# Optimization experiments

Measured on AMD Instinct MI355X. Metric: run time of the kernel, lower is better.

## Reference

```python
import jax, jax.numpy as jnp
import numpy as np

B = 32; H = 56; W = 56; C = 384; NH = 12; WS = 14; SS = 7
L = H * W; N = WS * WS; HD = C // NH; SCALE = HD ** -0.5; HID = 4 * C
NW = (H // WS) * (W // WS)
EPS = 1e-5

def _relative_index():
    ch = np.arange(WS)[:, None].repeat(WS, 1)
    cw = np.arange(WS)[None, :].repeat(WS, 0)
    coords = np.stack([ch, cw], -1).reshape(-1, 2)  # [N,2]
    rel = coords[:, None, :] - coords[None, :, :]
    rel = rel + (WS - 1)
    rel[:, :, 0] *= 2 * WS - 1
    return rel.sum(-1)  # [N,N], values in [0,(2WS-1)^2)

def _attn_mask():
    img = np.zeros((H, W))
    sl = (slice(0, -WS), slice(-WS, -SS), slice(-SS, None))
    cnt = 0
    for hs in sl:
        for ws_ in sl:
            img[hs, ws_] = cnt; cnt += 1
    mw = img.reshape(H // WS, WS, W // WS, WS).transpose(0, 2, 1, 3).reshape(-1, N)
    am = mw[:, None, :] - mw[:, :, None]  # [nW,N,N]
    return np.where(am != 0, -100.0, 0.0).astype(np.float32)

REL_IDX = jnp.asarray(_relative_index())
MASK = jnp.asarray(_attn_mask())  # [NW,N,N]

def _ln(x, w, b):
    m = jnp.mean(x, -1, keepdims=True)
    v = jnp.mean((x - m) ** 2, -1, keepdims=True)
    return (x - m) * jax.lax.rsqrt(v + EPS) * w + b

def setup_inputs() -> dict:
    key = jax.random.key(0)
    ks = jax.random.split(key, 8)
    s = 0.02
    return {
        "x": jax.random.normal(ks[0], (B, L, C), jnp.float32),
        "norm1_w": jnp.ones((C,), jnp.float32),
        "norm1_b": jnp.zeros((C,), jnp.float32),
        "qkv_w": jax.random.normal(ks[1], (3 * C, C), jnp.float32) * s,
        "qkv_b": jnp.zeros((3 * C,), jnp.float32),
        "proj_w": jax.random.normal(ks[2], (C, C), jnp.float32) * s,
        "proj_b": jnp.zeros((C,), jnp.float32),
        "relative_table": jax.random.normal(ks[3], ((2 * WS - 1) ** 2, 2 * NH), jnp.float32) * s,
        "norm2_w": jnp.ones((C,), jnp.float32),
        "norm2_b": jnp.zeros((C,), jnp.float32),
        "fc1_w": jax.random.normal(ks[4], (HID, C), jnp.float32) * s,
        "fc1_b": jnp.zeros((HID,), jnp.float32),
        "fc2_w": jax.random.normal(ks[5], (C, HID), jnp.float32) * s,
        "fc2_b": jnp.zeros((C,), jnp.float32),
    }

def reference(x, norm1_w, norm1_b, qkv_w, qkv_b, proj_w, proj_b,
              relative_table, norm2_w, norm2_b, fc1_w, fc1_b, fc2_w, fc2_b):
    shortcut = x
    xn = _ln(x, norm1_w, norm1_b).reshape(B, H, W, C)
    # cyclic shift + window partition -> [B*NW, N, C]
    xs = jnp.roll(xn, (-SS, -SS), (1, 2))
    xw = xs.reshape(B, H // WS, WS, W // WS, WS, C).transpose(0, 1, 3, 2, 4, 5).reshape(-1, N, C)
    B_ = B * NW
    qkv = (xw @ qkv_w.T + qkv_b).reshape(B_, N, 3, NH, HD).transpose(2, 0, 3, 1, 4)
    q, k, v = qkv[0] * SCALE, qkv[1], qkv[2]  # [B_,NH,N,HD]
    attn = jnp.einsum('bhnd,bhmd->bhnm', q, k)  # [B_,NH,N,N]
    rel = relative_table[REL_IDX]  # [N,N,2*NH]
    rel = rel.transpose(2, 0, 1)  # [2*NH,N,N]
    bias, rscale = rel[:NH], rel[NH:]
    attn = attn + bias[None]
    attn = attn.reshape(B, NW, NH, N, N) + MASK[None, :, None]
    attn = jax.nn.softmax(attn.reshape(B_, NH, N, N), axis=-1)
    attn = attn * rscale[None]  # multiplicative relative scale AFTER softmax
    out = jnp.einsum('bhnm,bhmd->bhnd', attn, v)
    out = out.transpose(0, 2, 1, 3).reshape(B_, N, C)
    out = out @ proj_w.T + proj_b
    # window reverse + reverse shift
    xr = out.reshape(B, H // WS, W // WS, WS, WS, C).transpose(0, 1, 3, 2, 4, 5).reshape(B, H, W, C)
    xr = jnp.roll(xr, (SS, SS), (1, 2)).reshape(B, L, C)
    x = shortcut + xr
    h = _ln(x, norm2_w, norm2_b)
    h = jax.nn.gelu(h @ fc1_w.T + fc1_b, approximate=False) @ fc2_w.T + fc2_b
    return x + h
```

## Files before the change

### kernel.cpp

```cpp
#include <hip/hip_runtime.h>
#include <hip/hip_bf16.h>
#include <math.h>

#define BDIM 32
#define HDIM 56
#define WDIM 56
#define CDIM 384
#define NHEAD 12
#define WSZ 14
#define SSZ 7
#define LDIM (HDIM*WDIM)
#define NTOK (WSZ*WSZ)
#define HDHEAD (CDIM/NHEAD)
#define HIDDIM (4*CDIM)
#define NWIN 16
#define BWIN (BDIM*NWIN)
#define MROWS (BDIM*LDIM)
#define EPSLN 1e-5f
#define ATTSCALE 0.17677669529663687f
#define QKVC (3*CDIM)

#define KROW 40
#define VROW 232
#define PROW 232

typedef __hip_bfloat16 bf16;
typedef __attribute__((ext_vector_type(8))) short bf16x8;
typedef __attribute__((ext_vector_type(4))) short s16x4;
typedef __attribute__((ext_vector_type(4))) float f32x4;

#define ASYNC16(gp, lp) __builtin_amdgcn_global_load_lds( \
    (__attribute__((address_space(1))) void*)(gp),        \
    (__attribute__((address_space(3))) void*)(lp), 16, 0, 0)

static __device__ __forceinline__ short f2bfs(float x) {
  union { bf16 h; short s; } u; u.h = __float2bfloat16(x); return u.s;
}
static __device__ __forceinline__ float bfs2f(short s) {
  unsigned int u = ((unsigned int)(unsigned short)s) << 16;
  float f; __builtin_memcpy(&f, &u, 4); return f;
}
static __device__ __forceinline__ float tof(float x) { return x; }
static __device__ __forceinline__ float tof(bf16 x)  { return __bfloat162float(x); }

__global__ __launch_bounds__(256) void k_cvt(const float* __restrict__ in,
                                             bf16* __restrict__ out, int n)
{
  int i = blockIdx.x * 256 + threadIdx.x;
  if (i < n) out[i] = __float2bfloat16(in[i]);
}

template<bool WIN, typename TIN>
__global__ __launch_bounds__(128) void k_ln(const TIN* __restrict__ xin,
    const float* __restrict__ gw, const float* __restrict__ gb,
    bf16* __restrict__ out)
{
  int r = blockIdx.x;
  int t = threadIdx.x;
  const TIN* xp = xin + (size_t)r * CDIM;
  float v0 = tof(xp[t]), v1 = tof(xp[t+128]), v2 = tof(xp[t+256]);
  float s  = v0+v1+v2;
  float ss = v0*v0 + v1*v1 + v2*v2;
  #pragma unroll
  for (int o = 32; o > 0; o >>= 1) { s += __shfl_down(s, o); ss += __shfl_down(ss, o); }
  __shared__ float red[4];
  if ((t & 63) == 0) { red[(t>>6)*2] = s; red[(t>>6)*2+1] = ss; }
  __syncthreads();
  float mean = (red[0]+red[2]) * (1.0f/CDIM);
  float var  = (red[1]+red[3]) * (1.0f/CDIM) - mean*mean;
  float rstd = rsqrtf(var + EPSLN);

  size_t orow;
  if (WIN) {
    int b = r / LDIM, l = r % LDIM;
    int h = l / WDIM, w = l % WDIM;
    int h2 = (h + HDIM - SSZ) % HDIM, w2 = (w + WDIM - SSZ) % WDIM;
    int wh = h2 / WSZ, ii = h2 % WSZ, ww = w2 / WSZ, jj = w2 % WSZ;
    int b_ = b*NWIN + wh*4 + ww;
    int n  = ii*WSZ + jj;
    orow = ((size_t)b_*NTOK + n) * CDIM;
  } else {
    orow = (size_t)r * CDIM;
  }
  out[orow+t]     = __float2bfloat16((v0-mean)*rstd*gw[t]     + gb[t]);
  out[orow+t+128] = __float2bfloat16((v1-mean)*rstd*gw[t+128] + gb[t+128]);
  out[orow+t+256] = __float2bfloat16((v2-mean)*rstd*gw[t+256] + gb[t+256]);
}

template<int KD, int EPI>
__global__ __launch_bounds__(512, 4) void k_mgemm(
    const bf16* __restrict__ A, const bf16* __restrict__ Wb,
    const float* __restrict__ bias, const float* __restrict__ aux,
    const bf16* __restrict__ auxb,
    float* __restrict__ outf, bf16* __restrict__ outb, int gx)
{
  __shared__ short As[256*64];
  __shared__ short Bs[128*64];
  int tid  = threadIdx.x;
  int lane = tid & 63, wid = tid >> 6;
  int c15 = lane & 15, h4 = lane >> 4;
  int wr = wid >> 1, wc = wid & 1;

  int nwg = gridDim.x, bid = blockIdx.x;
  int swz = (bid & 7) * (nwg >> 3) + (bid >> 3);
  int ty = swz / gx, tx = swz - ty * gx;
  int row0 = ty * 256, col0 = tx * 128;

  f32x4 acc[4][4] = {};

  int srow = lane >> 3;
  int skk  = ((lane & 7) ^ srow) * 8;

  const int NT = KD / 64;

  for (int t = 0; t < NT; t++) {
    int k0 = t * 64;
    #pragma unroll
    for (int s = 0; s < 4; s++) {
      int c = wid*4 + s;
      ASYNC16(A + (size_t)(row0 + c*8 + srow)*KD + k0 + skk, &As[c*512]);
    }
    #pragma unroll
    for (int s = 0; s < 2; s++) {
      int c = wid*2 + s;
      ASYNC16(Wb + (size_t)(col0 + c*8 + srow)*KD + k0 + skk, &Bs[c*512]);
    }
    __syncthreads();

    #pragma unroll
    for (int half = 0; half < 2; half++) {
      bf16x8 af[4], bfr[4];
      int blk8 = ((half << 2) + h4) ^ (c15 & 7);
      #pragma unroll
      for (int m = 0; m < 4; m++) {
        int rr = wr*64 + m*16 + c15;
        af[m] = *reinterpret_cast<const bf16x8*>(&As[rr*64 + blk8*8]);
      }
      #pragma unroll
      for (int n = 0; n < 4; n++) {
        int rr = wc*64 + n*16 + c15;
        bfr[n] = *reinterpret_cast<const bf16x8*>(&Bs[rr*64 + blk8*8]);
      }
      #pragma unroll
      for (int n = 0; n < 4; n++)
        #pragma unroll
        for (int m = 0; m < 4; m++)
          acc[n][m] = __builtin_amdgcn_mfma_f32_16x16x32_bf16(bfr[n], af[m], acc[n][m], 0, 0, 0);
    }
    __syncthreads();
  }

  int rb = row0 + wr*64 + c15;
  int cb = col0 + wc*64 + h4*4;
  #pragma unroll
  for (int m = 0; m < 4; m++) {
    int r = rb + m*16;
    if constexpr (EPI == 0) {
      #pragma unroll
      for (int n = 0; n < 4; n++) {
        int c0 = cb + n*16;
        f32x4 v = acc[n][m];
        f32x4 b4 = *(const f32x4*)&bias[c0];
        float scl = (c0 < CDIM) ? ATTSCALE : 1.f;
        s16x4 o;
        #pragma unroll
        for (int i = 0; i < 4; i++) o[i] = f2bfs((v[i] + b4[i]) * scl);
        *(s16x4*)&outb[(size_t)r*QKVC + c0] = o;
      }
    } else if constexpr (EPI == 1) {
      int b_ = r / NTOK, nn = r % NTOK;
      int b = b_ >> 4, wi = b_ & 15, wh = wi >> 2, ww = wi & 3;
      int ii = nn / WSZ, jj = nn % WSZ;
      int hh = (wh*WSZ + ii + SSZ) % HDIM;
      int wcc = (ww*WSZ + jj + SSZ) % WDIM;
      size_t rr = ((size_t)b*LDIM + hh*WDIM + wcc) * CDIM;
      #pragma unroll
      for (int n = 0; n < 4; n++) {
        int c0 = cb + n*16;
        f32x4 v = acc[n][m];
        f32x4 b4 = *(const f32x4*)&bias[c0];
        f32x4 a4 = *(const f32x4*)&aux[rr + c0];
        s16x4 o;
        #pragma unroll
        for (int i = 0; i < 4; i++) o[i] = f2bfs(a4[i] + v[i] + b4[i]);
        *(s16x4*)&outb[rr + c0] = o;
      }
    } else if constexpr (EPI == 2) {
      #pragma unroll
      for (int n = 0; n < 4; n++) {
        int c0 = cb + n*16;
        f32x4 v = acc[n][m];
        f32x4 b4 = *(const f32x4*)&bias[c0];
        s16x4 o;
        #pragma unroll
        for (int i = 0; i < 4; i++) {
          float val = v[i] + b4[i];
          val = 0.5f * val * (1.0f + erff(val * 0.70710678118654752f));
          o[i] = f2bfs(val);
        }
        *(s16x4*)&outb[(size_t)r*HIDDIM + c0] = o;
      }
    } else {
      #pragma unroll
      for (int n = 0; n < 4; n++) {
        int c0 = cb + n*16;
        f32x4 v = acc[n][m];
        f32x4 b4 = *(const f32x4*)&bias[c0];
        s16x4 ab = *(const s16x4*)&auxb[(size_t)r*CDIM + c0];
        f32x4 o;
        #pragma unroll
        for (int i = 0; i < 4; i++) o[i] = v[i] + b4[i] + bfs2f(ab[i]);
        *(f32x4*)&outf[(size_t)r*CDIM + c0] = o;
      }
    }
  }
}

__global__ __launch_bounds__(256) void k_attn_mfma(const bf16* __restrict__ qkv,
    const float* __restrict__ rt, bf16* __restrict__ out)
{
  __shared__ short  Ks[208*KROW];
  __shared__ short  Vt[32*VROW];
  __shared__ short  Ps[4][16*PROW];
  __shared__ float2 tab2[729];
  __shared__ int    regv[208];

  int blk = blockIdx.x;
  int b_ = blk / NHEAD, head = blk % NHEAD;
  int tid = threadIdx.x, lane = tid & 63, wid = tid >> 6;
  int c15 = lane & 15, h4 = lane >> 4;

  const bf16* rowbase = qkv + (size_t)b_*NTOK*QKVC + head*HDHEAD;
  const bf16* kp = rowbase + CDIM;
  const bf16* vp = rowbase + 2*CDIM;
  for (int c = tid; c < 784; c += 256) {
    int m = c >> 2, k8 = (c & 3) * 8;
    *(bf16x8*)&Ks[m*KROW + k8] = *(const bf16x8*)(kp + (size_t)m*QKVC + k8);
    bf16x8 vv = *(const bf16x8*)(vp + (size_t)m*QKVC + k8);
    #pragma unroll
    for (int j = 0; j < 8; j++) Vt[(k8+j)*VROW + m] = vv[j];
  }
  for (int e = tid; e < 12*KROW; e += 256) Ks[196*KROW + e] = 0;
  for (int e = tid; e < 32*28; e += 256) Vt[(e/28)*VROW + 196 + (e%28)] = 0;
  for (int e = tid; e < 729; e += 256)
    tab2[e] = make_float2(rt[e*2*NHEAD + head], rt[e*2*NHEAD + NHEAD + head]);
  {
    int wi = b_ & 15, wh = wi >> 2, ww = wi & 3;
    for (int e = tid; e < 208; e += 256) {
      int rv = 0;
      if (e < NTOK) {
        int i = e / WSZ, j = e % WSZ;
        int ha = wh*WSZ + i, wa = ww*WSZ + j;
        int rh = ha < (HDIM-WSZ) ? 0 : (ha < (HDIM-SSZ) ? 1 : 2);
        int rw = wa < (WDIM-WSZ) ? 0 : (wa < (WDIM-SSZ) ? 1 : 2);
        rv = rh*3 + rw;
      }
      regv[e] = rv;
    }
  }
  __syncthreads();

  int   moff[13], mreg[13];
  float mpad[13];
  #pragma unroll
  for (int t = 0; t < 13; t++) {
    int m  = t*16 + c15;
    int mm = min(m, NTOK-1);
    moff[t] = (mm/WSZ)*27 + (mm%WSZ);
    mreg[t] = regv[mm];
    mpad[t] = (m >= NTOK) ? -1e30f : 0.f;
  }

  short* myP = &Ps[wid][0];
  #pragma unroll
  for (int i = 0; i < 4; i++) myP[(h4*4+i)*PROW + 208 + c15] = 0;

  bf16* op = out + (size_t)b_*NTOK*CDIM + head*HDHEAD;

  for (int s = wid; s < 13; s += 4) {
    int qrow = min(s*16 + c15, NTOK-1);
    bf16x8 qf = *(const bf16x8*)(rowbase + (size_t)qrow*QKVC + h4*8);

    f32x4 sc[13];
    #pragma unroll
    for (int t = 0; t < 13; t++) {
      bf16x8 kf = *(const bf16x8*)&Ks[(t*16 + c15)*KROW + h4*8];
      sc[t] = __builtin_amdgcn_mfma_f32_16x16x32_bf16(qf, kf, (f32x4){0.f,0.f,0.f,0.f}, 0, 0, 0);
    }

    #pragma unroll
    for (int i = 0; i < 4; i++) {
      int n  = s*16 + h4*4 + i;
      int nc = min(n, NTOK-1);
      int nbase = ((nc/WSZ) + 13)*27 + (nc%WSZ) + 13;
      int nreg  = regv[nc];
      float rr[13];
      float sum = 0.f;
      #pragma unroll
      for (int t = 0; t < 13; t++) {
        float2 hr = tab2[nbase - moff[t]];
        float sv = sc[t][i] + hr.x + ((mreg[t] != nreg) ? -100.f : 0.f) + mpad[t];
        float e = __expf(sv);
        rr[t] = hr.y;
        sc[t][i] = e; sum += e;
      }
      #pragma unroll
      for (int o = 1; o < 16; o <<= 1) sum += __shfl_xor(sum, o);
      float inv = 1.f / sum;
      int prow = h4*4 + i;
      #pragma unroll
      for (int t = 0; t < 13; t++)
        myP[prow*PROW + t*16 + c15] = f2bfs(sc[t][i] * inv * rr[t]);
    }

    asm volatile("s_waitcnt lgkmcnt(0)" ::: "memory");
    __builtin_amdgcn_sched_barrier(0);

    f32x4 o0 = {0.f,0.f,0.f,0.f}, o1 = {0.f,0.f,0.f,0.f};
    #pragma unroll
    for (int t7 = 0; t7 < 7; t7++) {
      bf16x8 pf = *(const bf16x8*)&myP[c15*PROW + t7*32 + h4*8];
      bf16x8 v0 = *(const bf16x8*)&Vt[c15*VROW + t7*32 + h4*8];
      bf16x8 v1 = *(const bf16x8*)&Vt[(16 + c15)*VROW + t7*32 + h4*8];
      o0 = __builtin_amdgcn_mfma_f32_16x16x32_bf16(pf, v0, o0, 0, 0, 0);
      o1 = __builtin_amdgcn_mfma_f32_16x16x32_bf16(pf, v1, o1, 0, 0, 0);
    }

    #pragma unroll
    for (int i = 0; i < 4; i++) {
      int n = s*16 + h4*4 + i;
      if (n < NTOK) {
        op[(size_t)n*CDIM + c15]      = __float2bfloat16(o0[i]);
        op[(size_t)n*CDIM + 16 + c15] = __float2bfloat16(o1[i]);
      }
    }
  }
}

extern "C" void kernel_launch(void* const* d_in, const int* in_sizes, int n_in,
                              void* d_out, int out_size, void* d_ws, size_t ws_size,
                              hipStream_t stream)
{
  const float* x      = (const float*)d_in[0];
  const float* n1w    = (const float*)d_in[1];
  const float* n1b    = (const float*)d_in[2];
  const float* qkv_w  = (const float*)d_in[3];
  const float* qkv_b  = (const float*)d_in[4];
  const float* proj_w = (const float*)d_in[5];
  const float* proj_b = (const float*)d_in[6];
  const float* rt     = (const float*)d_in[7];
  const float* n2w    = (const float*)d_in[8];
  const float* n2b    = (const float*)d_in[9];
  const float* fc1_w  = (const float*)d_in[10];
  const float* fc1_b  = (const float*)d_in[11];
  const float* fc2_w  = (const float*)d_in[12];
  const float* fc2_b  = (const float*)d_in[13];

  char* ws = (char*)d_ws;
  const size_t SZ_BF = (size_t)MROWS * CDIM * 2;
  bf16*  xw      = (bf16*)ws;
  bf16*  attnout = (bf16*)ws;
  bf16*  qkv     = (bf16*)(ws + SZ_BF);
  bf16*  x2b     = (bf16*)(ws + SZ_BF);
  bf16*  hln     = (bf16*)(ws + 2*SZ_BF);
  bf16*  hid     = (bf16*)(ws + 4*SZ_BF);
  const int NQKVW = 3*CDIM*CDIM;
  const int NPROJW = CDIM*CDIM;
  const int NFCW  = HIDDIM*CDIM;
  bf16* wq  = (bf16*)(ws + 4*SZ_BF);
  bf16* wp  = wq + NQKVW;
  bf16* wf1 = (bf16*)ws;
  bf16* wf2 = wf1 + NFCW;

  k_cvt<<<(NQKVW+255)/256, 256, 0, stream>>>(qkv_w, wq, NQKVW);
  k_cvt<<<(NPROJW+255)/256, 256, 0, stream>>>(proj_w, wp, NPROJW);

  k_ln<true, float><<<MROWS, 128, 0, stream>>>(x, n1w, n1b, xw);
  k_mgemm<CDIM, 0><<<(MROWS/256)*9, 512, 0, stream>>>(
      xw, wq, qkv_b, nullptr, nullptr, nullptr, qkv, 9);
  k_attn_mfma<<<BWIN*NHEAD, 256, 0, stream>>>(qkv, rt, attnout);
  k_mgemm<CDIM, 1><<<(MROWS/256)*3, 512, 0, stream>>>(
      attnout, wp, proj_b, x, nullptr, nullptr, x2b, 3);

  k_cvt<<<(NFCW+255)/256, 256, 0, stream>>>(fc1_w, wf1, NFCW);
  k_cvt<<<(NFCW+255)/256, 256, 0, stream>>>(fc2_w, wf2, NFCW);

  k_ln<false, bf16><<<MROWS, 128, 0, stream>>>(x2b, n2w, n2b, hln);
  k_mgemm<CDIM, 2><<<(MROWS/256)*12, 512, 0, stream>>>(
      hln, wf1, fc1_b, nullptr, nullptr, nullptr, hid, 12);
  k_mgemm<HIDDIM, 3><<<(MROWS/256)*3, 512, 0, stream>>>(
      hid, wf2, fc2_b, nullptr, x2b, (float*)d_out, nullptr, 3);
}
```

Measured before the change: 1.035 ms.

## Precompute packed bias/mask/scale table and vectorize LayerNorm per wavefront

Adds a kernel that builds, per window position and head, a packed bf16 table holding relative bias plus shift mask (and -inf for padding) and the post-softmax scale. The attention kernel then reads this table from global memory instead of building per-block LDS tables and computing mask regions, and it reorders block ids so blocks that share a window position and head run close together. LayerNorm now handles one row per wavefront with vector loads and stores and a shuffle-only reduction, with no LDS or block barrier. The cost is a table of about 33 MB that is built each call and read through cache, plus reduced precision for the bias stored as bf16.

```diff
diff --git a/kernel.cpp b/kernel.cpp
--- a/kernel.cpp
+++ b/kernel.cpp
@@ -19,6 +19,7 @@
 #define EPSLN 1e-5f
 #define ATTSCALE 0.17677669529663687f
 #define QKVC (3*CDIM)
+#define TBLM 224
 
 #define KROW 40
 #define VROW 232
@@ -27,6 +28,7 @@
 typedef __hip_bfloat16 bf16;
 typedef __attribute__((ext_vector_type(8))) short bf16x8;
 typedef __attribute__((ext_vector_type(4))) short s16x4;
+typedef __attribute__((ext_vector_type(2))) short s16x2;
 typedef __attribute__((ext_vector_type(4))) float f32x4;
 
 #define ASYNC16(gp, lp) __builtin_amdgcn_global_load_lds( \
@@ -40,8 +42,6 @@
   unsigned int u = ((unsigned int)(unsigned short)s) << 16;
   float f; __builtin_memcpy(&f, &u, 4); return f;
 }
-static __device__ __forceinline__ float tof(float x) { return x; }
-static __device__ __forceinline__ float tof(bf16 x)  { return __bfloat162float(x); }
 
 __global__ __launch_bounds__(256) void k_cvt(const float* __restrict__ in,
                                              bf16* __restrict__ out, int n)
@@ -50,24 +50,66 @@
   if (i < n) out[i] = __float2bfloat16(in[i]);
 }
 
+__global__ __launch_bounds__(256) void k_btab(const float* __restrict__ rt,
+                                              unsigned int* __restrict__ tbl)
+{
+  int idx = blockIdx.x*256 + threadIdx.x;
+  int mp   = idx % TBLM;
+  int rest = idx / TBLM;
+  int n    = rest % NTOK;  rest /= NTOK;
+  int head = rest % NHEAD;
+  int wi   = rest / NHEAD;
+
+  unsigned int outv;
+  if (mp >= NTOK) {
+    outv = 0x0000FF80u;
+  } else {
+    int ni = n / WSZ,  nj = n % WSZ;
+    int mi = mp / WSZ, mj = mp % WSZ;
+    int ridx = (ni - mi + 13)*27 + (nj - mj + 13);
+    float bias = rt[ridx*2*NHEAD + head];
+    float rsc  = rt[ridx*2*NHEAD + NHEAD + head];
+    int wh = wi >> 2, ww = wi & 3;
+    int ha = wh*WSZ + ni, wa = ww*WSZ + nj;
+    int rn = (ha < (HDIM-WSZ) ? 0 : (ha < (HDIM-SSZ) ? 1 : 2))*3
+           + (wa < (WDIM-WSZ) ? 0 : (wa < (WDIM-SSZ) ? 1 : 2));
+    int hb = wh*WSZ + mi, wb = ww*WSZ + mj;
+    int rm = (hb < (HDIM-WSZ) ? 0 : (hb < (HDIM-SSZ) ? 1 : 2))*3
+           + (wb < (WDIM-WSZ) ? 0 : (wb < (WDIM-SSZ) ? 1 : 2));
+    if (rn != rm) bias -= 100.f;
+    unsigned int lo = (unsigned short)f2bfs(bias);
+    unsigned int hi = (unsigned short)f2bfs(rsc);
+    outv = lo | (hi << 16);
+  }
+  tbl[idx] = outv;
+}
+
 template<bool WIN, typename TIN>
-__global__ __launch_bounds__(128) void k_ln(const TIN* __restrict__ xin,
+__global__ __launch_bounds__(256) void k_ln(const TIN* __restrict__ xin,
     const float* __restrict__ gw, const float* __restrict__ gb,
     bf16* __restrict__ out)
 {
-  int r = blockIdx.x;
-  int t = threadIdx.x;
+  int lane = threadIdx.x & 63, wid = threadIdx.x >> 6;
+  int r = blockIdx.x*4 + wid;
   const TIN* xp = xin + (size_t)r * CDIM;
-  float v0 = tof(xp[t]), v1 = tof(xp[t+128]), v2 = tof(xp[t+256]);
-  float s  = v0+v1+v2;
-  float ss = v0*v0 + v1*v1 + v2*v2;
+  float v[6];
+  if constexpr (sizeof(TIN) == 4) {
+    float4 a = *(const float4*)((const float*)xp + lane*4);
+    float2 b = *(const float2*)((const float*)xp + 256 + lane*2);
+    v[0]=a.x; v[1]=a.y; v[2]=a.z; v[3]=a.w; v[4]=b.x; v[5]=b.y;
+  } else {
+    s16x4 a = *(const s16x4*)((const short*)xp + lane*4);
+    s16x2 b = *(const s16x2*)((const short*)xp + 256 + lane*2);
+    v[0]=bfs2f(a[0]); v[1]=bfs2f(a[1]); v[2]=bfs2f(a[2]); v[3]=bfs2f(a[3]);
+    v[4]=bfs2f(b[0]); v[5]=bfs2f(b[1]);
+  }
+  float s = 0.f, ss = 0.f;
   #pragma unroll
-  for (int o = 32; o > 0; o >>= 1) { s += __shfl_down(s, o); ss += __shfl_down(ss, o); }
-  __shared__ float red[4];
-  if ((t & 63) == 0) { red[(t>>6)*2] = s; red[(t>>6)*2+1] = ss; }
-  __syncthreads();
-  float mean = (red[0]+red[2]) * (1.0f/CDIM);
-  float var  = (red[1]+red[3]) * (1.0f/CDIM) - mean*mean;
+  for (int j = 0; j < 6; j++) { s += v[j]; ss += v[j]*v[j]; }
+  #pragma unroll
+  for (int o = 1; o < 64; o <<= 1) { s += __shfl_xor(s, o); ss += __shfl_xor(ss, o); }
+  float mean = s * (1.0f/CDIM);
+  float var  = ss * (1.0f/CDIM) - mean*mean;
   float rstd = rsqrtf(var + EPSLN);
 
   size_t orow;
@@ -82,9 +124,20 @@
   } else {
     orow = (size_t)r * CDIM;
   }
-  out[orow+t]     = __float2bfloat16((v0-mean)*rstd*gw[t]     + gb[t]);
-  out[orow+t+128] = __float2bfloat16((v1-mean)*rstd*gw[t+128] + gb[t+128]);
-  out[orow+t+256] = __float2bfloat16((v2-mean)*rstd*gw[t+256] + gb[t+256]);
+  float4 w4 = *(const float4*)(gw + lane*4);
+  float2 w2 = *(const float2*)(gw + 256 + lane*2);
+  float4 g4 = *(const float4*)(gb + lane*4);
+  float2 g2 = *(const float2*)(gb + 256 + lane*2);
+  s16x4 o4;
+  o4[0] = f2bfs((v[0]-mean)*rstd*w4.x + g4.x);
+  o4[1] = f2bfs((v[1]-mean)*rstd*w4.y + g4.y);
+  o4[2] = f2bfs((v[2]-mean)*rstd*w4.z + g4.z);
+  o4[3] = f2bfs((v[3]-mean)*rstd*w4.w + g4.w);
+  *(s16x4*)((short*)out + orow + lane*4) = o4;
+  s16x2 o2;
+  o2[0] = f2bfs((v[4]-mean)*rstd*w2.x + g2.x);
+  o2[1] = f2bfs((v[5]-mean)*rstd*w2.y + g2.y);
+  *(s16x2*)((short*)out + orow + 256 + lane*2) = o2;
 }
 
 template<int KD, int EPI>
@@ -217,15 +270,14 @@
 }
 
 __global__ __launch_bounds__(256) void k_attn_mfma(const bf16* __restrict__ qkv,
-    const float* __restrict__ rt, bf16* __restrict__ out)
+    const unsigned int* __restrict__ tbl, bf16* __restrict__ out)
 {
   __shared__ short  Ks[208*KROW];
   __shared__ short  Vt[32*VROW];
   __shared__ short  Ps[4][16*PROW];
-  __shared__ float2 tab2[729];
-  __shared__ int    regv[208];
-
-  int blk = blockIdx.x;
+
+  int bid = blockIdx.x;
+  int blk = (bid & 7) * 768 + (bid >> 3);
   int b_ = blk / NHEAD, head = blk % NHEAD;
   int tid = threadIdx.x, lane = tid & 63, wid = tid >> 6;
   int c15 = lane & 15, h4 = lane >> 4;
@@ -242,34 +294,9 @@
   }
   for (int e = tid; e < 12*KROW; e += 256) Ks[196*KROW + e] = 0;
   for (int e = tid; e < 32*28; e += 256) Vt[(e/28)*VROW + 196 + (e%28)] = 0;
-  for (int e = tid; e < 729; e += 256)
-    tab2[e] = make_float2(rt[e*2*NHEAD + head], rt[e*2*NHEAD + NHEAD + head]);
-  {
-    int wi = b_ & 15, wh = wi >> 2, ww = wi & 3;
-    for (int e = tid; e < 208; e += 256) {
-      int rv = 0;
-      if (e < NTOK) {
-        int i = e / WSZ, j = e % WSZ;
-        int ha = wh*WSZ + i, wa = ww*WSZ + j;
-        int rh = ha < (HDIM-WSZ) ? 0 : (ha < (HDIM-SSZ) ? 1 : 2);
-        int rw = wa < (WDIM-WSZ) ? 0 : (wa < (WDIM-SSZ) ? 1 : 2);
-        rv = rh*3 + rw;
-      }
-      regv[e] = rv;
-    }
-  }
   __syncthreads();
 
-  int   moff[13], mreg[13];
-  float mpad[13];
-  #pragma unroll
-  for (int t = 0; t < 13; t++) {
-    int m  = t*16 + c15;
-    int mm = min(m, NTOK-1);
-    moff[t] = (mm/WSZ)*27 + (mm%WSZ);
-    mreg[t] = regv[mm];
-    mpad[t] = (m >= NTOK) ? -1e30f : 0.f;
-  }
+  const unsigned int* tblbh = tbl + (size_t)((b_ & 15)*NHEAD + head)*NTOK*TBLM;
 
   short* myP = &Ps[wid][0];
   #pragma unroll
@@ -291,18 +318,16 @@
     #pragma unroll
     for (int i = 0; i < 4; i++) {
       int n  = s*16 + h4*4 + i;
-      int nc = min(n, NTOK-1);
-      int nbase = ((nc/WSZ) + 13)*27 + (nc%WSZ) + 13;
-      int nreg  = regv[nc];
-      float rr[13];
+      int ncl = min(n, NTOK-1);
+      const unsigned int* trow = tblbh + (size_t)ncl*TBLM;
       float sum = 0.f;
       #pragma unroll
       for (int t = 0; t < 13; t++) {
-        float2 hr = tab2[nbase - moff[t]];
-        float sv = sc[t][i] + hr.x + ((mreg[t] != nreg) ? -100.f : 0.f) + mpad[t];
-        float e = __expf(sv);
-        rr[t] = hr.y;
-        sc[t][i] = e; sum += e;
+        unsigned int tv = trow[t*16 + c15];
+        float bv = bfs2f((short)(tv & 0xFFFFu));
+        float e = __expf(sc[t][i] + bv);
+        sum += e;
+        sc[t][i] = e * bfs2f((short)(tv >> 16));
       }
       #pragma unroll
       for (int o = 1; o < 16; o <<= 1) sum += __shfl_xor(sum, o);
@@ -310,7 +335,7 @@
       int prow = h4*4 + i;
       #pragma unroll
       for (int t = 0; t < 13; t++)
-        myP[prow*PROW + t*16 + c15] = f2bfs(sc[t][i] * inv * rr[t]);
+        myP[prow*PROW + t*16 + c15] = f2bfs(sc[t][i] * inv);
     }
 
     asm volatile("s_waitcnt lgkmcnt(0)" ::: "memory");
@@ -371,21 +396,23 @@
   bf16* wp  = wq + NQKVW;
   bf16* wf1 = (bf16*)ws;
   bf16* wf2 = wf1 + NFCW;
+  unsigned int* tbl = (unsigned int*)(ws + 5*SZ_BF);
 
   k_cvt<<<(NQKVW+255)/256, 256, 0, stream>>>(qkv_w, wq, NQKVW);
   k_cvt<<<(NPROJW+255)/256, 256, 0, stream>>>(proj_w, wp, NPROJW);
-
-  k_ln<true, float><<<MROWS, 128, 0, stream>>>(x, n1w, n1b, xw);
+  k_btab<<<(NWIN*NHEAD*NTOK*TBLM)/256, 256, 0, stream>>>(rt, tbl);
+
+  k_ln<true, float><<<MROWS/4, 256, 0, stream>>>(x, n1w, n1b, xw);
   k_mgemm<CDIM, 0><<<(MROWS/256)*9, 512, 0, stream>>>(
       xw, wq, qkv_b, nullptr, nullptr, nullptr, qkv, 9);
-  k_attn_mfma<<<BWIN*NHEAD, 256, 0, stream>>>(qkv, rt, attnout);
+  k_attn_mfma<<<BWIN*NHEAD, 256, 0, stream>>>(qkv, tbl, attnout);
   k_mgemm<CDIM, 1><<<(MROWS/256)*3, 512, 0, stream>>>(
       attnout, wp, proj_b, x, nullptr, nullptr, x2b, 3);
 
   k_cvt<<<(NFCW+255)/256, 256, 0, stream>>>(fc1_w, wf1, NFCW);
   k_cvt<<<(NFCW+255)/256, 256, 0, stream>>>(fc2_w, wf2, NFCW);
 
-  k_ln<false, bf16><<<MROWS, 128, 0, stream>>>(x2b, n2w, n2b, hln);
+  k_ln<false, bf16><<<MROWS/4, 256, 0, stream>>>(x2b, n2w, n2b, hln);
   k_mgemm<CDIM, 2><<<(MROWS/256)*12, 512, 0, stream>>>(
       hln, wf1, fc1_b, nullptr, nullptr, nullptr, hid, 12);
   k_mgemm<HIDDIM, 3><<<(MROWS/256)*3, 512, 0, stream>>>(
```

Result: no change. 1.033 ms (-0.3%).

## Double-buffer GEMM K-tiles with async prefetch and use one-wave-per-row LayerNorm

Applied to the files above, without the earlier changes.

The GEMM now uses BK=32 with two LDS buffers and prefetches the next K-tile via global_load_lds. It waits with vmcnt(3) so the loads overlap the MFMAs on the current tile, and it uses a new XOR swizzle for the 32-wide rows. LayerNorm is rewritten so each 64-lane wave handles one row, with vectorized loads and stores and a shuffle-only reduction, removing the shared-memory reduction and __syncthreads. The risks are that the smaller K-tile doubles the number of barriers per K, and the manual vmcnt counting must match the exact number of issued loads.

```diff
diff --git a/kernel.cpp b/kernel.cpp
--- a/kernel.cpp
+++ b/kernel.cpp
@@ -27,6 +27,7 @@
 typedef __hip_bfloat16 bf16;
 typedef __attribute__((ext_vector_type(8))) short bf16x8;
 typedef __attribute__((ext_vector_type(4))) short s16x4;
+typedef __attribute__((ext_vector_type(2))) short s16x2;
 typedef __attribute__((ext_vector_type(4))) float f32x4;
 
 #define ASYNC16(gp, lp) __builtin_amdgcn_global_load_lds( \
@@ -40,8 +41,6 @@
   unsigned int u = ((unsigned int)(unsigned short)s) << 16;
   float f; __builtin_memcpy(&f, &u, 4); return f;
 }
-static __device__ __forceinline__ float tof(float x) { return x; }
-static __device__ __forceinline__ float tof(bf16 x)  { return __bfloat162float(x); }
 
 __global__ __launch_bounds__(256) void k_cvt(const float* __restrict__ in,
                                              bf16* __restrict__ out, int n)
@@ -51,23 +50,31 @@
 }
 
 template<bool WIN, typename TIN>
-__global__ __launch_bounds__(128) void k_ln(const TIN* __restrict__ xin,
+__global__ __launch_bounds__(256) void k_ln(const TIN* __restrict__ xin,
     const float* __restrict__ gw, const float* __restrict__ gb,
     bf16* __restrict__ out)
 {
-  int r = blockIdx.x;
-  int t = threadIdx.x;
+  int lane = threadIdx.x & 63, wid = threadIdx.x >> 6;
+  int r = blockIdx.x*4 + wid;
   const TIN* xp = xin + (size_t)r * CDIM;
-  float v0 = tof(xp[t]), v1 = tof(xp[t+128]), v2 = tof(xp[t+256]);
-  float s  = v0+v1+v2;
-  float ss = v0*v0 + v1*v1 + v2*v2;
+  float v[6];
+  if constexpr (sizeof(TIN) == 4) {
+    float4 a = *(const float4*)((const float*)xp + lane*4);
+    float2 b = *(const float2*)((const float*)xp + 256 + lane*2);
+    v[0]=a.x; v[1]=a.y; v[2]=a.z; v[3]=a.w; v[4]=b.x; v[5]=b.y;
+  } else {
+    s16x4 a = *(const s16x4*)((const short*)xp + lane*4);
+    s16x2 b = *(const s16x2*)((const short*)xp + 256 + lane*2);
+    v[0]=bfs2f(a[0]); v[1]=bfs2f(a[1]); v[2]=bfs2f(a[2]); v[3]=bfs2f(a[3]);
+    v[4]=bfs2f(b[0]); v[5]=bfs2f(b[1]);
+  }
+  float s = 0.f, ss = 0.f;
   #pragma unroll
-  for (int o = 32; o > 0; o >>= 1) { s += __shfl_down(s, o); ss += __shfl_down(ss, o); }
-  __shared__ float red[4];
-  if ((t & 63) == 0) { red[(t>>6)*2] = s; red[(t>>6)*2+1] = ss; }
-  __syncthreads();
-  float mean = (red[0]+red[2]) * (1.0f/CDIM);
-  float var  = (red[1]+red[3]) * (1.0f/CDIM) - mean*mean;
+  for (int j = 0; j < 6; j++) { s += v[j]; ss += v[j]*v[j]; }
+  #pragma unroll
+  for (int o = 1; o < 64; o <<= 1) { s += __shfl_xor(s, o); ss += __shfl_xor(ss, o); }
+  float mean = s * (1.0f/CDIM);
+  float var  = ss * (1.0f/CDIM) - mean*mean;
   float rstd = rsqrtf(var + EPSLN);
 
   size_t orow;
@@ -82,9 +89,20 @@
   } else {
     orow = (size_t)r * CDIM;
   }
-  out[orow+t]     = __float2bfloat16((v0-mean)*rstd*gw[t]     + gb[t]);
-  out[orow+t+128] = __float2bfloat16((v1-mean)*rstd*gw[t+128] + gb[t+128]);
-  out[orow+t+256] = __float2bfloat16((v2-mean)*rstd*gw[t+256] + gb[t+256]);
+  float4 w4 = *(const float4*)(gw + lane*4);
+  float2 w2 = *(const float2*)(gw + 256 + lane*2);
+  float4 g4 = *(const float4*)(gb + lane*4);
+  float2 g2 = *(const float2*)(gb + 256 + lane*2);
+  s16x4 o4;
+  o4[0] = f2bfs((v[0]-mean)*rstd*w4.x + g4.x);
+  o4[1] = f2bfs((v[1]-mean)*rstd*w4.y + g4.y);
+  o4[2] = f2bfs((v[2]-mean)*rstd*w4.z + g4.z);
+  o4[3] = f2bfs((v[3]-mean)*rstd*w4.w + g4.w);
+  *(s16x4*)((short*)out + orow + lane*4) = o4;
+  s16x2 o2;
+  o2[0] = f2bfs((v[4]-mean)*rstd*w2.x + g2.x);
+  o2[1] = f2bfs((v[5]-mean)*rstd*w2.y + g2.y);
+  *(s16x2*)((short*)out + orow + 256 + lane*2) = o2;
 }
 
 template<int KD, int EPI>
@@ -94,8 +112,8 @@
     const bf16* __restrict__ auxb,
     float* __restrict__ outf, bf16* __restrict__ outb, int gx)
 {
-  __shared__ short As[256*64];
-  __shared__ short Bs[128*64];
+  __shared__ short As[2][256*32];
+  __shared__ short Bs[2][128*32];
   int tid  = threadIdx.x;
   int lane = tid & 63, wid = tid >> 6;
   int c15 = lane & 15, h4 = lane >> 4;
@@ -108,47 +126,49 @@
 
   f32x4 acc[4][4] = {};
 
-  int srow = lane >> 3;
-  int skk  = ((lane & 7) ^ srow) * 8;
-
-  const int NT = KD / 64;
+  int r0  = tid >> 2, b0 = tid & 3;
+  int sk0 = (b0 ^ (r0 & 3) ^ ((r0 >> 2) & 3)) * 8;
+
+  const int NT = KD / 32;
+
+#define STAGE_T(k0, bf) do { \
+    ASYNC16(A  + (size_t)(row0 + r0)*KD       + (k0) + sk0, &As[bf][tid*8]); \
+    ASYNC16(A  + (size_t)(row0 + r0 + 128)*KD + (k0) + sk0, &As[bf][(tid+512)*8]); \
+    ASYNC16(Wb + (size_t)(col0 + r0)*KD       + (k0) + sk0, &Bs[bf][tid*8]); \
+  } while (0)
+
+  STAGE_T(0, 0);
+
+  int rblk = (h4 ^ (c15 & 3) ^ ((c15 >> 2) & 3)) * 8;
 
   for (int t = 0; t < NT; t++) {
-    int k0 = t * 64;
-    #pragma unroll
-    for (int s = 0; s < 4; s++) {
-      int c = wid*4 + s;
-      ASYNC16(A + (size_t)(row0 + c*8 + srow)*KD + k0 + skk, &As[c*512]);
-    }
-    #pragma unroll
-    for (int s = 0; s < 2; s++) {
-      int c = wid*2 + s;
-      ASYNC16(Wb + (size_t)(col0 + c*8 + srow)*KD + k0 + skk, &Bs[c*512]);
-    }
-    __syncthreads();
-
-    #pragma unroll
-    for (int half = 0; half < 2; half++) {
-      bf16x8 af[4], bfr[4];
-      int blk8 = ((half << 2) + h4) ^ (c15 & 7);
-      #pragma unroll
-      for (int m = 0; m < 4; m++) {
-        int rr = wr*64 + m*16 + c15;
-        af[m] = *reinterpret_cast<const bf16x8*>(&As[rr*64 + blk8*8]);
-      }
-      #pragma unroll
-      for (int n = 0; n < 4; n++) {
-        int rr = wc*64 + n*16 + c15;
-        bfr[n] = *reinterpret_cast<const bf16x8*>(&Bs[rr*64 + blk8*8]);
-      }
-      #pragma unroll
-      for (int n = 0; n < 4; n++)
-        #pragma unroll
-        for (int m = 0; m < 4; m++)
-          acc[n][m] = __builtin_amdgcn_mfma_f32_16x16x32_bf16(bfr[n], af[m], acc[n][m], 0, 0, 0);
-    }
-    __syncthreads();
-  }
+    int cur = t & 1;
+    if (t + 1 < NT) {
+      STAGE_T((t+1)*32, cur^1);
+      asm volatile("s_waitcnt vmcnt(3)" ::: "memory");
+    } else {
+      asm volatile("s_waitcnt vmcnt(0)" ::: "memory");
+    }
+    __builtin_amdgcn_s_barrier();
+    __builtin_amdgcn_sched_barrier(0);
+
+    bf16x8 af[4], bfr[4];
+    #pragma unroll
+    for (int m = 0; m < 4; m++)
+      af[m] = *reinterpret_cast<const bf16x8*>(&As[cur][(wr*64 + m*16 + c15)*32 + rblk]);
+    #pragma unroll
+    for (int n = 0; n < 4; n++)
+      bfr[n] = *reinterpret_cast<const bf16x8*>(&Bs[cur][(wc*64 + n*16 + c15)*32 + rblk]);
+    #pragma unroll
+    for (int n = 0; n < 4; n++)
+      #pragma unroll
+      for (int m = 0; m < 4; m++)
+        acc[n][m] = __builtin_amdgcn_mfma_f32_16x16x32_bf16(bfr[n], af[m], acc[n][m], 0, 0, 0);
+
+    __builtin_amdgcn_sched_barrier(0);
+    __builtin_amdgcn_s_barrier();
+  }
+#undef STAGE_T
 
   int rb = row0 + wr*64 + c15;
   int cb = col0 + wc*64 + h4*4;
@@ -375,7 +395,7 @@
   k_cvt<<<(NQKVW+255)/256, 256, 0, stream>>>(qkv_w, wq, NQKVW);
   k_cvt<<<(NPROJW+255)/256, 256, 0, stream>>>(proj_w, wp, NPROJW);
 
-  k_ln<true, float><<<MROWS, 128, 0, stream>>>(x, n1w, n1b, xw);
+  k_ln<true, float><<<MROWS/4, 256, 0, stream>>>(x, n1w, n1b, xw);
   k_mgemm<CDIM, 0><<<(MROWS/256)*9, 512, 0, stream>>>(
       xw, wq, qkv_b, nullptr, nullptr, nullptr, qkv, 9);
   k_attn_mfma<<<BWIN*NHEAD, 256, 0, stream>>>(qkv, rt, attnout);
@@ -385,7 +405,7 @@
   k_cvt<<<(NFCW+255)/256, 256, 0, stream>>>(fc1_w, wf1, NFCW);
   k_cvt<<<(NFCW+255)/256, 256, 0, stream>>>(fc2_w, wf2, NFCW);
 
-  k_ln<false, bf16><<<MROWS, 128, 0, stream>>>(x2b, n2w, n2b, hln);
+  k_ln<false, bf16><<<MROWS/4, 256, 0, stream>>>(x2b, n2w, n2b, hln);
   k_mgemm<CDIM, 2><<<(MROWS/256)*12, 512, 0, stream>>>(
       hln, wf1, fc1_b, nullptr, nullptr, nullptr, hid, 12);
   k_mgemm<HIDDIM, 3><<<(MROWS/256)*3, 512, 0, stream>>>(
```

Measured after the change: 1.012 ms. 1.02x faster.
